# Performance work log

Measured on AMD Instinct MI355X. Metric: run time of the kernel, lower is better.

## Reference

```python
import jax, jax.numpy as jnp
import numpy as np

VOCAB, EMBED, HID = 32000, 512, 1024
B, S = 64, 512


def setup_inputs() -> dict:
    key = jax.random.key(0)
    ks = jax.random.split(key, 14)
    sc = lambda fan: 1.0 / np.sqrt(fan)
    return {
        "input_token": jax.random.randint(ks[0], (B, 1), 0, VOCAB),
        "h": jax.random.normal(ks[1], (1, B, HID), jnp.float32),
        "c": jax.random.normal(ks[2], (1, B, HID), jnp.float32),
        "encoder_outputs": jax.random.normal(ks[3], (B, S, HID), jnp.float32),
        "emb": jax.random.normal(ks[4], (VOCAB, EMBED), jnp.float32).at[0].set(0.0),
        "W1": jax.random.normal(ks[5], (HID, HID), jnp.float32) * sc(HID),
        "W2": jax.random.normal(ks[6], (HID, HID), jnp.float32) * sc(HID),
        "v": jax.random.normal(ks[7], (HID,), jnp.float32) * sc(HID),
        "W_ih": jax.random.normal(ks[8], (4 * HID, EMBED + HID), jnp.float32) * sc(EMBED + HID),
        "W_hh": jax.random.normal(ks[9], (4 * HID, HID), jnp.float32) * sc(HID),
        "b_ih": jax.random.normal(ks[10], (4 * HID,), jnp.float32) * 0.01,
        "b_hh": jax.random.normal(ks[11], (4 * HID,), jnp.float32) * 0.01,
        "fc_W": jax.random.normal(ks[12], (VOCAB, 2 * HID), jnp.float32) * sc(2 * HID),
        "fc_b": jax.random.normal(ks[13], (VOCAB,), jnp.float32) * 0.01,
    }


def reference(input_token, h, c, encoder_outputs, emb, W1, W2, v,
              W_ih, W_hh, b_ih, b_hh, fc_W, fc_b):
    # Embedding (dropout = identity in eval)
    embedded = emb[input_token[:, 0]]                       # [B, E]
    h0 = h[0]                                               # [B, H]
    c0 = c[0]                                               # [B, H]

    # Bahdanau additive attention
    dh = h0 @ W1.T                                          # [B, H]
    eh = jnp.einsum('bsh,kh->bsk', encoder_outputs, W2)     # [B, S, H]
    energy = jnp.tanh(dh[:, None, :] + eh)                  # [B, S, H]
    scores = jnp.einsum('bsh,h->bs', energy, v)             # [B, S]
    attn = jax.nn.softmax(scores, axis=-1)                  # [B, S]
    context = jnp.einsum('bs,bsh->bh', attn, encoder_outputs)  # [B, H]

    # Single LSTM step (PyTorch gate order: i, f, g, o)
    x = jnp.concatenate([embedded, context], axis=-1)       # [B, E+H]
    gates = x @ W_ih.T + b_ih + h0 @ W_hh.T + b_hh          # [B, 4H]
    i, f, g, o = jnp.split(gates, 4, axis=-1)
    c1 = jax.nn.sigmoid(f) * c0 + jax.nn.sigmoid(i) * jnp.tanh(g)
    h1 = jax.nn.sigmoid(o) * jnp.tanh(c1)                   # [B, H]

    # Output projection
    out = jnp.concatenate([h1, context], axis=-1)           # [B, 2H]
    prediction = out @ fc_W.T + fc_b                        # [B, V]
    return prediction, (h1[None], c1[None]), attn
```

## Files before the change

### kernel.cpp

```cpp
#include <hip/hip_runtime.h>
#include <math.h>

#define VOCAB 32000
#define EMBED 512
#define HID   1024
#define BATCH 64
#define SEQ   512

#define OUT_H1   2048000
#define OUT_C1   2113536
#define OUT_ATTN 2179072

typedef __bf16 bf16x8 __attribute__((ext_vector_type(8)));
typedef float  f32x4  __attribute__((ext_vector_type(4)));

__device__ __forceinline__ unsigned short f2bf(float f) {
  unsigned int u = __builtin_bit_cast(unsigned int, f);
  u += 0x7fffu + ((u >> 16) & 1u);
  return (unsigned short)(u >> 16);
}
__device__ __forceinline__ float bf2f(unsigned int u) {
  return __builtin_bit_cast(float, u << 16);
}

__device__ __forceinline__ float fast_tanh(float x) {
  float cx = fminf(fmaxf(x, -15.f), 15.f);
  float t = __builtin_amdgcn_exp2f(cx * 2.8853900817779268f);
  return (t - 1.f) / (t + 1.f);
}

__device__ __forceinline__ void gload16(const unsigned short* g, unsigned short* l) {
  __builtin_amdgcn_global_load_lds(
      (const __attribute__((address_space(1))) void*)g,
      (__attribute__((address_space(3))) void*)l, 16, 0, 0);
}

__device__ __forceinline__ void stage16(const float* __restrict__ src, unsigned short* dst) {
  float4 f0 = *(const float4*)(src + 0);
  float4 f1 = *(const float4*)(src + 4);
  float4 f2 = *(const float4*)(src + 8);
  float4 f3 = *(const float4*)(src + 12);
  union { unsigned short us[16]; uint4 u4[2]; } p;
  p.us[0]=f2bf(f0.x);  p.us[1]=f2bf(f0.y);  p.us[2]=f2bf(f0.z);  p.us[3]=f2bf(f0.w);
  p.us[4]=f2bf(f1.x);  p.us[5]=f2bf(f1.y);  p.us[6]=f2bf(f1.z);  p.us[7]=f2bf(f1.w);
  p.us[8]=f2bf(f2.x);  p.us[9]=f2bf(f2.y);  p.us[10]=f2bf(f2.z); p.us[11]=f2bf(f2.w);
  p.us[12]=f2bf(f3.x); p.us[13]=f2bf(f3.y); p.us[14]=f2bf(f3.z); p.us[15]=f2bf(f3.w);
  *(uint4*)(dst + 0) = p.u4[0];
  *(uint4*)(dst + 8) = p.u4[1];
}

__global__ void zero_ws_kernel(float* __restrict__ p) {
  int i = blockIdx.x * 256 + threadIdx.x;
  *(float4*)(p + (size_t)i * 4) = (float4){0.f, 0.f, 0.f, 0.f};
}

__global__ void f2bf_kernel(const float* __restrict__ src, unsigned short* __restrict__ dst,
                            int n8) {
  int i = blockIdx.x * blockDim.x + threadIdx.x;
  int stride = gridDim.x * blockDim.x;
  for (; i < n8; i += stride) {
    const float* s = src + (size_t)i * 8;
    float4 f0 = *(const float4*)s;
    float4 f1 = *(const float4*)(s + 4);
    union { unsigned short us[8]; uint4 u; } p;
    p.us[0]=f2bf(f0.x); p.us[1]=f2bf(f0.y); p.us[2]=f2bf(f0.z); p.us[3]=f2bf(f0.w);
    p.us[4]=f2bf(f1.x); p.us[5]=f2bf(f1.y); p.us[6]=f2bf(f1.z); p.us[7]=f2bf(f1.w);
    *(uint4*)(dst + (size_t)i * 8) = p.u;
  }
}

__global__ void dh_kernel(const float* __restrict__ h0, const float* __restrict__ W1,
                          float* __restrict__ dh) {
  __shared__ float hs[HID];
  int b = blockIdx.y, t = threadIdx.x;
  for (int i = t; i < HID; i += 256) hs[i] = h0[b * HID + i];
  __syncthreads();
  int k = blockIdx.x * 256 + t;
  const float* w = W1 + (size_t)k * HID;
  float acc = 0.f;
  for (int hh = 0; hh < HID; hh += 4) {
    float4 wv = *(const float4*)(w + hh);
    float4 hv = *(const float4*)(hs + hh);
    acc += wv.x * hv.x + wv.y * hv.y + wv.z * hv.z + wv.w * hv.w;
  }
  dh[b * HID + k] = acc;
}

__launch_bounds__(512, 2)
__global__ void scores8_kernel(const unsigned short* __restrict__ encb,
                               const unsigned short* __restrict__ W2b,
                               const float* __restrict__ dh, const float* __restrict__ v,
                               float* __restrict__ scores) {
  __shared__ __align__(16) unsigned short sA[2][16384];
  __shared__ __align__(16) unsigned short sB[2][16384];
  __shared__ float dh_s[256];
  __shared__ float v_s[256];

  int bid = blockIdx.x;
  int wg = (bid & 7) * 64 + (bid >> 3);
  int mt = wg >> 2, nt = wg & 3;
  int m0 = mt * 256, n0 = nt * 256;

  int t = threadIdx.x;
  int wid = t >> 6, l = t & 63;
  int wr = wid >> 2, wc = wid & 3;
  int fr = l & 15, co = (l >> 4) * 8;

  const unsigned short* pa0;
  const unsigned short* pb0;
  int do0 = wid * 512;
  {
    int base = wid * 1024 + l * 16;
    int srel = base ^ (((base >> 8) & 3) << 4);
    int row = srel >> 7, colE = (srel >> 1) & 63;
    pa0 = encb + (size_t)(m0 + row) * HID + colE;
    pb0 = W2b + (size_t)(n0 + row) * HID + colE;
  }

  f32x4 acc[8][4];
#pragma unroll
  for (int i = 0; i < 8; i++)
#pragma unroll
    for (int j = 0; j < 4; j++) acc[i][j] = (f32x4){0.f, 0.f, 0.f, 0.f};

#define SC_STAGE(T, d)                                                         \
  do {                                                                         \
    int k0_ = (T) * 64;                                                        \
    gload16(pa0 + k0_,          &sA[d][do0]);                                  \
    gload16(pa0 + 65536 + k0_,  &sA[d][do0 + 4096]);                           \
    gload16(pa0 + 131072 + k0_, &sA[d][do0 + 8192]);                           \
    gload16(pa0 + 196608 + k0_, &sA[d][do0 + 12288]);                          \
    gload16(pb0 + k0_,          &sB[d][do0]);                                  \
    gload16(pb0 + 65536 + k0_,  &sB[d][do0 + 4096]);                           \
    gload16(pb0 + 131072 + k0_, &sB[d][do0 + 8192]);                           \
    gload16(pb0 + 196608 + k0_, &sB[d][do0 + 12288]);                          \
  } while (0)

  SC_STAGE(0, 0);
  SC_STAGE(1, 1);

#define LDF(Mat, row, ks) \
  (*(const bf16x8*)&Mat[(row) * 64 + (((ks) * 32 + co) ^ ((((row) >> 1) & 3) << 3))])

  for (int T = 0; T < 16; ++T) {
    int d = T & 1;
    if (T == 15) asm volatile("s_waitcnt vmcnt(0)" ::: "memory");
    else         asm volatile("s_waitcnt vmcnt(8)" ::: "memory");
    asm volatile("s_barrier" ::: "memory");
    const unsigned short* A = sA[d];
    const unsigned short* B = sB[d];
    bf16x8 a[4][2], b[4][2];
#pragma unroll
    for (int jj = 0; jj < 4; ++jj)
#pragma unroll
      for (int ks = 0; ks < 2; ++ks)
        b[jj][ks] = LDF(B, wc * 64 + jj * 16 + fr, ks);
#pragma unroll
    for (int ii = 0; ii < 4; ++ii)
#pragma unroll
      for (int ks = 0; ks < 2; ++ks)
        a[ii][ks] = LDF(A, wr * 128 + ii * 16 + fr, ks);
    __builtin_amdgcn_s_setprio(1);
#pragma unroll
    for (int ii = 0; ii < 4; ++ii)
#pragma unroll
      for (int jj = 0; jj < 2; ++jj)
#pragma unroll
        for (int ks = 0; ks < 2; ++ks)
          acc[ii][jj] = __builtin_amdgcn_mfma_f32_16x16x32_bf16(a[ii][ks], b[jj][ks], acc[ii][jj], 0, 0, 0);
    __builtin_amdgcn_s_setprio(0);
    __builtin_amdgcn_s_setprio(1);
#pragma unroll
    for (int ii = 0; ii < 4; ++ii)
#pragma unroll
      for (int jj = 2; jj < 4; ++jj)
#pragma unroll
        for (int ks = 0; ks < 2; ++ks)
          acc[ii][jj] = __builtin_amdgcn_mfma_f32_16x16x32_bf16(a[ii][ks], b[jj][ks], acc[ii][jj], 0, 0, 0);
    __builtin_amdgcn_s_setprio(0);
#pragma unroll
    for (int ii = 0; ii < 4; ++ii)
#pragma unroll
      for (int ks = 0; ks < 2; ++ks)
        a[ii][ks] = LDF(A, wr * 128 + 64 + ii * 16 + fr, ks);
    __builtin_amdgcn_s_setprio(1);
#pragma unroll
    for (int ii = 0; ii < 4; ++ii)
#pragma unroll
      for (int jj = 2; jj < 4; ++jj)
#pragma unroll
        for (int ks = 0; ks < 2; ++ks)
          acc[4 + ii][jj] = __builtin_amdgcn_mfma_f32_16x16x32_bf16(a[ii][ks], b[jj][ks], acc[4 + ii][jj], 0, 0, 0);
    __builtin_amdgcn_s_setprio(0);
    __builtin_amdgcn_s_setprio(1);
#pragma unroll
    for (int ii = 0; ii < 4; ++ii)
#pragma unroll
      for (int jj = 0; jj < 2; ++jj)
#pragma unroll
        for (int ks = 0; ks < 2; ++ks)
          acc[4 + ii][jj] = __builtin_amdgcn_mfma_f32_16x16x32_bf16(a[ii][ks], b[jj][ks], acc[4 + ii][jj], 0, 0, 0);
    __builtin_amdgcn_s_setprio(0);
    asm volatile("s_barrier" ::: "memory");
    if (T < 14) SC_STAGE(T + 2, d);
  }
#undef LDF
#undef SC_STAGE

  int b = m0 >> 9;
  if (t < 256) { dh_s[t] = dh[b * HID + n0 + t]; v_s[t] = v[n0 + t]; }
  __syncthreads();
  float sp[32];
#pragma unroll
  for (int q = 0; q < 32; ++q) sp[q] = 0.f;
#pragma unroll
  for (int ii = 0; ii < 8; ++ii)
#pragma unroll
    for (int jj = 0; jj < 4; ++jj) {
      int nl = wc * 64 + jj * 16 + fr;
      float dv = dh_s[nl], vv = v_s[nl];
#pragma unroll
      for (int r = 0; r < 4; ++r)
        sp[ii * 4 + r] += fast_tanh(dv + acc[ii][jj][r]) * vv;
    }
#pragma unroll
  for (int q = 0; q < 32; ++q) {
    float x = sp[q];
    x += __shfl_xor(x, 1);
    x += __shfl_xor(x, 2);
    x += __shfl_xor(x, 4);
    x += __shfl_xor(x, 8);
    sp[q] = x;
  }
  if (fr == 0) {
    int rbase = m0 + wr * 128 + (l >> 4) * 4;
#pragma unroll
    for (int ii = 0; ii < 8; ++ii)
#pragma unroll
      for (int r = 0; r < 4; ++r)
        atomicAdd(&scores[rbase + ii * 16 + r], sp[ii * 4 + r]);
  }
}

__global__ void softmax_kernel(const float* __restrict__ scores, float* __restrict__ attn) {
  __shared__ float red[8];
  int b = blockIdx.x, t = threadIdx.x;
  float x = scores[b * SEQ + t];
  float m = x;
  for (int d = 1; d < 64; d <<= 1) m = fmaxf(m, __shfl_xor(m, d));
  if ((t & 63) == 0) red[t >> 6] = m;
  __syncthreads();
  float bm = red[0];
#pragma unroll
  for (int i = 1; i < 8; i++) bm = fmaxf(bm, red[i]);
  float e = expf(x - bm);
  float s = e;
  for (int d = 1; d < 64; d <<= 1) s += __shfl_xor(s, d);
  __syncthreads();
  if ((t & 63) == 0) red[t >> 6] = s;
  __syncthreads();
  float bs = 0.f;
#pragma unroll
  for (int i = 0; i < 8; i++) bs += red[i];
  attn[b * SEQ + t] = e / bs;
}

__global__ void context2_kernel(const unsigned short* __restrict__ encb,
                                const float* __restrict__ attn, float* __restrict__ ctx) {
  __shared__ float a_s[64];
  int b = blockIdx.y, s0 = blockIdx.x * 64, t = threadIdx.x;
  if (t < 64) a_s[t] = attn[b * SEQ + s0 + t];
  __syncthreads();
  int hg = (t & 127) * 8, sg = (t >> 7) * 32;
  float a0 = 0.f, a1 = 0.f, a2 = 0.f, a3 = 0.f, a4 = 0.f, a5 = 0.f, a6 = 0.f, a7 = 0.f;
  const unsigned short* base = encb + ((size_t)b * SEQ + s0 + sg) * HID + hg;
  for (int s = 0; s < 32; s++) {
    uint4 ev = *(const uint4*)(base + (size_t)s * HID);
    float a = a_s[sg + s];
    a0 += a * bf2f(ev.x & 0xffffu); a1 += a * bf2f(ev.x >> 16);
    a2 += a * bf2f(ev.y & 0xffffu); a3 += a * bf2f(ev.y >> 16);
    a4 += a * bf2f(ev.z & 0xffffu); a5 += a * bf2f(ev.z >> 16);
    a6 += a * bf2f(ev.w & 0xffffu); a7 += a * bf2f(ev.w >> 16);
  }
  atomicAdd(&ctx[b * HID + hg + 0], a0);
  atomicAdd(&ctx[b * HID + hg + 1], a1);
  atomicAdd(&ctx[b * HID + hg + 2], a2);
  atomicAdd(&ctx[b * HID + hg + 3], a3);
  atomicAdd(&ctx[b * HID + hg + 4], a4);
  atomicAdd(&ctx[b * HID + hg + 5], a5);
  atomicAdd(&ctx[b * HID + hg + 6], a6);
  atomicAdd(&ctx[b * HID + hg + 7], a7);
}

__launch_bounds__(256)
__global__ void gates8p_kernel(const int* __restrict__ tok, const float* __restrict__ emb,
                               const float* __restrict__ ctx, const float* __restrict__ h0,
                               const float* __restrict__ W_ih, const float* __restrict__ W_hh,
                               float* __restrict__ gpart) {
  __shared__ __align__(16) unsigned short lA[64 * 40];
  __shared__ __align__(16) unsigned short lB[128 * 40];
  int n0 = blockIdx.x * 128, kz = blockIdx.y;
  int kbase = kz * 320;
  int t = threadIdx.x, w = t >> 6, l = t & 63;
  f32x4 acc[4][2];
#pragma unroll
  for (int i = 0; i < 4; i++)
#pragma unroll
    for (int j = 0; j < 2; j++) acc[i][j] = (f32x4){0.f, 0.f, 0.f, 0.f};
  int rowA = t >> 2, qA = (t & 3) * 8;
  int rowB = t >> 1, hB = t & 1;
  int tkA = tok[rowA];

  for (int kt = 0; kt < 10; kt++) {
    int k0 = kbase + kt * 32;
    {
      int kg = k0 + qA;
      const float* src;
      if (kg < 512)        src = emb + (size_t)tkA * EMBED + kg;
      else if (kg < 1536)  src = ctx + rowA * HID + (kg - 512);
      else                 src = h0 + rowA * HID + (kg - 1536);
      float4 f0 = *(const float4*)src;
      float4 f1 = *(const float4*)(src + 4);
      union { unsigned short us[8]; uint4 u; } p;
      p.us[0]=f2bf(f0.x); p.us[1]=f2bf(f0.y); p.us[2]=f2bf(f0.z); p.us[3]=f2bf(f0.w);
      p.us[4]=f2bf(f1.x); p.us[5]=f2bf(f1.y); p.us[6]=f2bf(f1.z); p.us[7]=f2bf(f1.w);
      *(uint4*)&lA[rowA * 40 + qA] = p.u;
    }
    {
      int kg = k0 + hB * 16;
      const float* src = (kg < 1536) ? (W_ih + (size_t)(n0 + rowB) * 1536 + kg)
                                     : (W_hh + (size_t)(n0 + rowB) * 1024 + (kg - 1536));
      stage16(src, &lB[rowB * 40 + hB * 16]);
    }
    __syncthreads();
    bf16x8 af[4], bv[2];
    int co = (l >> 4) * 8;
#pragma unroll
    for (int i = 0; i < 4; i++) af[i] = *(const bf16x8*)&lA[(i * 16 + (l & 15)) * 40 + co];
#pragma unroll
    for (int j = 0; j < 2; j++) bv[j] = *(const bf16x8*)&lB[(w * 32 + j * 16 + (l & 15)) * 40 + co];
#pragma unroll
    for (int i = 0; i < 4; i++)
#pragma unroll
      for (int j = 0; j < 2; j++)
        acc[i][j] = __builtin_amdgcn_mfma_f32_16x16x32_bf16(af[i], bv[j], acc[i][j], 0, 0, 0);
    __syncthreads();
  }
#pragma unroll
  for (int i = 0; i < 4; i++)
#pragma unroll
    for (int j = 0; j < 2; j++) {
      int n = n0 + w * 32 + j * 16 + (l & 15);
#pragma unroll
      for (int r = 0; r < 4; r++) {
        int m = i * 16 + (l >> 4) * 4 + r;
        gpart[(size_t)kz * 262144 + (size_t)m * 4096 + n] = acc[i][j][r];
      }
    }
}

__global__ void lstm_kernel(const float* __restrict__ gpart, const float* __restrict__ b_ih,
                            const float* __restrict__ b_hh, const float* __restrict__ c0,
                            float* __restrict__ out) {
  int b = blockIdx.y;
  int hh = blockIdx.x * 256 + threadIdx.x;
  float gi = b_ih[hh]        + b_hh[hh];
  float gf = b_ih[1024 + hh] + b_hh[1024 + hh];
  float gg = b_ih[2048 + hh] + b_hh[2048 + hh];
  float go = b_ih[3072 + hh] + b_hh[3072 + hh];
#pragma unroll
  for (int kz = 0; kz < 8; kz++) {
    const float* g = gpart + (size_t)kz * 262144 + (size_t)b * 4096;
    gi += g[hh];
    gf += g[1024 + hh];
    gg += g[2048 + hh];
    go += g[3072 + hh];
  }
  float si = 1.f / (1.f + expf(-gi));
  float sf = 1.f / (1.f + expf(-gf));
  float so = 1.f / (1.f + expf(-go));
  float c1 = sf * c0[b * HID + hh] + si * tanhf(gg);
  float h1 = so * tanhf(c1);
  out[OUT_H1 + b * HID + hh] = h1;
  out[OUT_C1 + b * HID + hh] = c1;
}

__launch_bounds__(256)
__global__ void fc2p_kernel(const float* __restrict__ h1, const float* __restrict__ ctx,
                            const float* __restrict__ fcW, float* __restrict__ part) {
  __shared__ __align__(16) unsigned short lA[64 * 40];
  __shared__ __align__(16) unsigned short lB[128 * 40];
  int n0 = blockIdx.x * 128, kz = blockIdx.y;
  const float* A = kz ? ctx : h1;
  int t = threadIdx.x, w = t >> 6, l = t & 63;
  f32x4 acc[4][2];
#pragma unroll
  for (int i = 0; i < 4; i++)
#pragma unroll
    for (int j = 0; j < 2; j++) acc[i][j] = (f32x4){0.f, 0.f, 0.f, 0.f};
  int rowA = t >> 2, qA = (t & 3) * 8;
  int rowB = t >> 1, hB = t & 1;

  for (int kt = 0; kt < 32; kt++) {
    int k0 = kt * 32;
    {
      const float* src = A + rowA * HID + k0 + qA;
      float4 f0 = *(const float4*)src;
      float4 f1 = *(const float4*)(src + 4);
      union { unsigned short us[8]; uint4 u; } p;
      p.us[0]=f2bf(f0.x); p.us[1]=f2bf(f0.y); p.us[2]=f2bf(f0.z); p.us[3]=f2bf(f0.w);
      p.us[4]=f2bf(f1.x); p.us[5]=f2bf(f1.y); p.us[6]=f2bf(f1.z); p.us[7]=f2bf(f1.w);
      *(uint4*)&lA[rowA * 40 + qA] = p.u;
    }
    stage16(fcW + (size_t)(n0 + rowB) * 2048 + kz * 1024 + k0 + hB * 16,
            &lB[rowB * 40 + hB * 16]);
    __syncthreads();
    bf16x8 af[4], bv[2];
    int co = (l >> 4) * 8;
#pragma unroll
    for (int i = 0; i < 4; i++) af[i] = *(const bf16x8*)&lA[(i * 16 + (l & 15)) * 40 + co];
#pragma unroll
    for (int j = 0; j < 2; j++) bv[j] = *(const bf16x8*)&lB[(w * 32 + j * 16 + (l & 15)) * 40 + co];
#pragma unroll
    for (int i = 0; i < 4; i++)
#pragma unroll
      for (int j = 0; j < 2; j++)
        acc[i][j] = __builtin_amdgcn_mfma_f32_16x16x32_bf16(af[i], bv[j], acc[i][j], 0, 0, 0);
    __syncthreads();
  }
#pragma unroll
  for (int i = 0; i < 4; i++)
#pragma unroll
    for (int j = 0; j < 2; j++) {
      int n = n0 + w * 32 + j * 16 + (l & 15);
#pragma unroll
      for (int r = 0; r < 4; r++) {
        int m = i * 16 + (l >> 4) * 4 + r;
        part[(size_t)kz * 2048000 + (size_t)m * VOCAB + n] = acc[i][j][r];
      }
    }
}

__global__ void fc_combine_kernel(const float* __restrict__ part,
                                  const float* __restrict__ fcb, float* __restrict__ pred) {
  int n = blockIdx.x * 256 + threadIdx.x;
  int m = blockIdx.y;
  size_t i = (size_t)m * VOCAB + n;
  pred[i] = part[i] + part[2048000 + i] + fcb[n];
}

extern "C" void kernel_launch(void* const* d_in, const int* in_sizes, int n_in,
                              void* d_out, int out_size, void* d_ws, size_t ws_size,
                              hipStream_t stream) {
  const int*   tok  = (const int*)d_in[0];
  const float* h    = (const float*)d_in[1];
  const float* c    = (const float*)d_in[2];
  const float* enc  = (const float*)d_in[3];
  const float* emb  = (const float*)d_in[4];
  const float* W1   = (const float*)d_in[5];
  const float* W2   = (const float*)d_in[6];
  const float* v    = (const float*)d_in[7];
  const float* W_ih = (const float*)d_in[8];
  const float* W_hh = (const float*)d_in[9];
  const float* b_ih = (const float*)d_in[10];
  const float* b_hh = (const float*)d_in[11];
  const float* fcW  = (const float*)d_in[12];
  const float* fcb  = (const float*)d_in[13];
  float* out = (float*)d_out;

  float* wsf    = (float*)d_ws;
  float* scores = wsf;
  float* ctx    = wsf + 32768;
  float* dh     = wsf + 98304;
  float* gpart  = wsf + 163840;
  float* part   = wsf + 2260992;
  unsigned short* encb = (unsigned short*)(wsf + 6356992);
  unsigned short* W2b  = encb + (size_t)BATCH * SEQ * HID;

  zero_ws_kernel<<<96, 256, 0, stream>>>(wsf);

  f2bf_kernel<<<2048, 256, 0, stream>>>(enc, encb, BATCH * SEQ * HID / 8);
  f2bf_kernel<<<512, 256, 0, stream>>>(W2, W2b, HID * HID / 8);
  dh_kernel<<<dim3(4, 64), 256, 0, stream>>>(h, W1, dh);
  scores8_kernel<<<512, 512, 0, stream>>>(encb, W2b, dh, v, scores);
  softmax_kernel<<<64, 512, 0, stream>>>(scores, out + OUT_ATTN);
  context2_kernel<<<dim3(8, 64), 256, 0, stream>>>(encb, out + OUT_ATTN, ctx);
  gates8p_kernel<<<dim3(32, 8), 256, 0, stream>>>(tok, emb, ctx, h, W_ih, W_hh, gpart);
  lstm_kernel<<<dim3(4, 64), 256, 0, stream>>>(gpart, b_ih, b_hh, c, out);
  fc2p_kernel<<<dim3(250, 2), 256, 0, stream>>>(out + OUT_H1, ctx, fcW, part);
  fc_combine_kernel<<<dim3(125, 64), 256, 0, stream>>>(part, fcb, out);
}
```

Measured before the change: 292.2 us.

## Fuse prep kernels, double-buffer fc LDS with register prefetch, vectorize combine

Merges the workspace zeroing, the enc and W2 bf16 conversions and the dh matvec into one launch that dispatches on block index, which cuts three kernel launches. The fc projection kernel now double-buffers its LDS tiles and prefetches the next k-slice into registers, so one barrier per iteration is dropped and global loads overlap the MFMAs. The combine kernel switches to float4 loads and stores. The changes add register pressure in fc2p, and the branches in the fused prep kernel diverge only at block granularity.

Measured after the change: 329.1 us. +12.7%, slower.

```diff
diff --git a/kernel.cpp b/kernel.cpp
--- a/kernel.cpp
+++ b/kernel.cpp
@@ -49,41 +49,51 @@
   *(uint4*)(dst + 8) = p.u4[1];
 }
 
-__global__ void zero_ws_kernel(float* __restrict__ p) {
-  int i = blockIdx.x * 256 + threadIdx.x;
-  *(float4*)(p + (size_t)i * 4) = (float4){0.f, 0.f, 0.f, 0.f};
-}
-
-__global__ void f2bf_kernel(const float* __restrict__ src, unsigned short* __restrict__ dst,
-                            int n8) {
-  int i = blockIdx.x * blockDim.x + threadIdx.x;
-  int stride = gridDim.x * blockDim.x;
-  for (; i < n8; i += stride) {
-    const float* s = src + (size_t)i * 8;
+__global__ void prep_kernel(const float* __restrict__ enc, unsigned short* __restrict__ encb,
+                            const float* __restrict__ W2, unsigned short* __restrict__ W2b,
+                            float* __restrict__ zr,
+                            const float* __restrict__ h0, const float* __restrict__ W1,
+                            float* __restrict__ dh) {
+  __shared__ float hs[HID];
+  int bid = blockIdx.x, t = threadIdx.x;
+  if (bid < 2048) {
+    int i = bid * 256 + t;
+    for (; i < BATCH * SEQ * HID / 8; i += 2048 * 256) {
+      const float* s = enc + (size_t)i * 8;
+      float4 f0 = *(const float4*)s;
+      float4 f1 = *(const float4*)(s + 4);
+      union { unsigned short us[8]; uint4 u; } p;
+      p.us[0]=f2bf(f0.x); p.us[1]=f2bf(f0.y); p.us[2]=f2bf(f0.z); p.us[3]=f2bf(f0.w);
+      p.us[4]=f2bf(f1.x); p.us[5]=f2bf(f1.y); p.us[6]=f2bf(f1.z); p.us[7]=f2bf(f1.w);
+      *(uint4*)(encb + (size_t)i * 8) = p.u;
+    }
+  } else if (bid < 2560) {
+    int i = (bid - 2048) * 256 + t;
+    const float* s = W2 + (size_t)i * 8;
     float4 f0 = *(const float4*)s;
     float4 f1 = *(const float4*)(s + 4);
     union { unsigned short us[8]; uint4 u; } p;
     p.us[0]=f2bf(f0.x); p.us[1]=f2bf(f0.y); p.us[2]=f2bf(f0.z); p.us[3]=f2bf(f0.w);
     p.us[4]=f2bf(f1.x); p.us[5]=f2bf(f1.y); p.us[6]=f2bf(f1.z); p.us[7]=f2bf(f1.w);
-    *(uint4*)(dst + (size_t)i * 8) = p.u;
-  }
-}
-
-__global__ void dh_kernel(const float* __restrict__ h0, const float* __restrict__ W1,
-                          float* __restrict__ dh) {
-  __shared__ float hs[HID];
-  int b = blockIdx.y, t = threadIdx.x;
-  for (int i = t; i < HID; i += 256) hs[i] = h0[b * HID + i];
-  __syncthreads();
-  int k = blockIdx.x * 256 + t;
-  const float* w = W1 + (size_t)k * HID;
-  float acc = 0.f;
-  for (int hh = 0; hh < HID; hh += 4) {
-    float4 wv = *(const float4*)(w + hh);
-    float4 hv = *(const float4*)(hs + hh);
-    acc += wv.x * hv.x + wv.y * hv.y + wv.z * hv.z + wv.w * hv.w;
-  }
-  dh[b * HID + k] = acc;
+    *(uint4*)(W2b + (size_t)i * 8) = p.u;
+  } else if (bid < 2656) {
+    int i = (bid - 2560) * 256 + t;
+    *(float4*)(zr + (size_t)i * 4) = (float4){0.f, 0.f, 0.f, 0.f};
+  } else {
+    int bb = bid - 2656;
+    int b = bb >> 2, kblk = bb & 3;
+    for (int i = t; i < HID; i += 256) hs[i] = h0[b * HID + i];
+    __syncthreads();
+    int k = kblk * 256 + t;
+    const float* w = W1 + (size_t)k * HID;
+    float acc = 0.f;
+    for (int hh = 0; hh < HID; hh += 4) {
+      float4 wv = *(const float4*)(w + hh);
+      float4 hv = *(const float4*)(hs + hh);
+      acc += wv.x * hv.x + wv.y * hv.y + wv.z * hv.z + wv.w * hv.w;
+    }
+    dh[b * HID + k] = acc;
+  }
 }
 
 __launch_bounds__(512, 2)
@@ -388,8 +398,8 @@
 __launch_bounds__(256)
 __global__ void fc2p_kernel(const float* __restrict__ h1, const float* __restrict__ ctx,
                             const float* __restrict__ fcW, float* __restrict__ part) {
-  __shared__ __align__(16) unsigned short lA[64 * 40];
-  __shared__ __align__(16) unsigned short lB[128 * 40];
+  __shared__ __align__(16) unsigned short lA[2][64 * 40];
+  __shared__ __align__(16) unsigned short lB[2][128 * 40];
   int n0 = blockIdx.x * 128, kz = blockIdx.y;
   const float* A = kz ? ctx : h1;
   int t = threadIdx.x, w = t >> 6, l = t & 63;
@@ -400,33 +410,46 @@
     for (int j = 0; j < 2; j++) acc[i][j] = (f32x4){0.f, 0.f, 0.f, 0.f};
   int rowA = t >> 2, qA = (t & 3) * 8;
   int rowB = t >> 1, hB = t & 1;
+  const float* asrc = A + rowA * HID + qA;
+  const float* bsrc = fcW + (size_t)(n0 + rowB) * 2048 + kz * 1024 + hB * 16;
+
+  float4 br0 = *(const float4*)(bsrc + 0), br1 = *(const float4*)(bsrc + 4);
+  float4 br2 = *(const float4*)(bsrc + 8), br3 = *(const float4*)(bsrc + 12);
+  float4 ar0 = *(const float4*)(asrc + 0), ar1 = *(const float4*)(asrc + 4);
 
   for (int kt = 0; kt < 32; kt++) {
-    int k0 = kt * 32;
+    int d = kt & 1;
     {
-      const float* src = A + rowA * HID + k0 + qA;
-      float4 f0 = *(const float4*)src;
-      float4 f1 = *(const float4*)(src + 4);
-      union { unsigned short us[8]; uint4 u; } p;
-      p.us[0]=f2bf(f0.x); p.us[1]=f2bf(f0.y); p.us[2]=f2bf(f0.z); p.us[3]=f2bf(f0.w);
-      p.us[4]=f2bf(f1.x); p.us[5]=f2bf(f1.y); p.us[6]=f2bf(f1.z); p.us[7]=f2bf(f1.w);
-      *(uint4*)&lA[rowA * 40 + qA] = p.u;
-    }
-    stage16(fcW + (size_t)(n0 + rowB) * 2048 + kz * 1024 + k0 + hB * 16,
-            &lB[rowB * 40 + hB * 16]);
+      union { unsigned short us[16]; uint4 u4[2]; } p;
+      p.us[0]=f2bf(br0.x);  p.us[1]=f2bf(br0.y);  p.us[2]=f2bf(br0.z);  p.us[3]=f2bf(br0.w);
+      p.us[4]=f2bf(br1.x);  p.us[5]=f2bf(br1.y);  p.us[6]=f2bf(br1.z);  p.us[7]=f2bf(br1.w);
+      p.us[8]=f2bf(br2.x);  p.us[9]=f2bf(br2.y);  p.us[10]=f2bf(br2.z); p.us[11]=f2bf(br2.w);
+      p.us[12]=f2bf(br3.x); p.us[13]=f2bf(br3.y); p.us[14]=f2bf(br3.z); p.us[15]=f2bf(br3.w);
+      *(uint4*)&lB[d][rowB * 40 + hB * 16 + 0] = p.u4[0];
+      *(uint4*)&lB[d][rowB * 40 + hB * 16 + 8] = p.u4[1];
+      union { unsigned short us[8]; uint4 u; } q;
+      q.us[0]=f2bf(ar0.x); q.us[1]=f2bf(ar0.y); q.us[2]=f2bf(ar0.z); q.us[3]=f2bf(ar0.w);
+      q.us[4]=f2bf(ar1.x); q.us[5]=f2bf(ar1.y); q.us[6]=f2bf(ar1.z); q.us[7]=f2bf(ar1.w);
+      *(uint4*)&lA[d][rowA * 40 + qA] = q.u;
+    }
+    if (kt < 31) {
+      int k1 = (kt + 1) * 32;
+      br0 = *(const float4*)(bsrc + k1 + 0);  br1 = *(const float4*)(bsrc + k1 + 4);
+      br2 = *(const float4*)(bsrc + k1 + 8);  br3 = *(const float4*)(bsrc + k1 + 12);
+      ar0 = *(const float4*)(asrc + k1 + 0);  ar1 = *(const float4*)(asrc + k1 + 4);
+    }
     __syncthreads();
     bf16x8 af[4], bv[2];
     int co = (l >> 4) * 8;
 #pragma unroll
-    for (int i = 0; i < 4; i++) af[i] = *(const bf16x8*)&lA[(i * 16 + (l & 15)) * 40 + co];
-#pragma unroll
-    for (int j = 0; j < 2; j++) bv[j] = *(const bf16x8*)&lB[(w * 32 + j * 16 + (l & 15)) * 40 + co];
+    for (int i = 0; i < 4; i++) af[i] = *(const bf16x8*)&lA[d][(i * 16 + (l & 15)) * 40 + co];
+#pragma unroll
+    for (int j = 0; j < 2; j++) bv[j] = *(const bf16x8*)&lB[d][(w * 32 + j * 16 + (l & 15)) * 40 + co];
 #pragma unroll
     for (int i = 0; i < 4; i++)
 #pragma unroll
       for (int j = 0; j < 2; j++)
         acc[i][j] = __builtin_amdgcn_mfma_f32_16x16x32_bf16(af[i], bv[j], acc[i][j], 0, 0, 0);
-    __syncthreads();
   }
 #pragma unroll
   for (int i = 0; i < 4; i++)
@@ -443,10 +466,18 @@
 
 __global__ void fc_combine_kernel(const float* __restrict__ part,
                                   const float* __restrict__ fcb, float* __restrict__ pred) {
-  int n = blockIdx.x * 256 + threadIdx.x;
-  int m = blockIdx.y;
-  size_t i = (size_t)m * VOCAB + n;
-  pred[i] = part[i] + part[2048000 + i] + fcb[n];
+  int i = blockIdx.x * 256 + threadIdx.x;
+  int m = i / 8000, n4 = i % 8000;
+  size_t e = (size_t)m * VOCAB + n4 * 4;
+  float4 p0 = *(const float4*)(part + e);
+  float4 p1 = *(const float4*)(part + 2048000 + e);
+  float4 bb = *(const float4*)(fcb + n4 * 4);
+  float4 o;
+  o.x = p0.x + p1.x + bb.x;
+  o.y = p0.y + p1.y + bb.y;
+  o.z = p0.z + p1.z + bb.z;
+  o.w = p0.w + p1.w + bb.w;
+  *(float4*)(pred + e) = o;
 }
 
 extern "C" void kernel_launch(void* const* d_in, const int* in_sizes, int n_in,
@@ -477,16 +508,12 @@
   unsigned short* encb = (unsigned short*)(wsf + 6356992);
   unsigned short* W2b  = encb + (size_t)BATCH * SEQ * HID;
 
-  zero_ws_kernel<<<96, 256, 0, stream>>>(wsf);
-
-  f2bf_kernel<<<2048, 256, 0, stream>>>(enc, encb, BATCH * SEQ * HID / 8);
-  f2bf_kernel<<<512, 256, 0, stream>>>(W2, W2b, HID * HID / 8);
-  dh_kernel<<<dim3(4, 64), 256, 0, stream>>>(h, W1, dh);
+  prep_kernel<<<2912, 256, 0, stream>>>(enc, encb, W2, W2b, wsf, h, W1, dh);
   scores8_kernel<<<512, 512, 0, stream>>>(encb, W2b, dh, v, scores);
   softmax_kernel<<<64, 512, 0, stream>>>(scores, out + OUT_ATTN);
   context2_kernel<<<dim3(8, 64), 256, 0, stream>>>(encb, out + OUT_ATTN, ctx);
   gates8p_kernel<<<dim3(32, 8), 256, 0, stream>>>(tok, emb, ctx, h, W_ih, W_hh, gpart);
   lstm_kernel<<<dim3(4, 64), 256, 0, stream>>>(gpart, b_ih, b_hh, c, out);
   fc2p_kernel<<<dim3(250, 2), 256, 0, stream>>>(out + OUT_H1, ctx, fcW, part);
-  fc_combine_kernel<<<dim3(125, 64), 256, 0, stream>>>(part, fcb, out);
-}
+  fc_combine_kernel<<<2000, 256, 0, stream>>>(part, fcb, out);
+}
```
